# Kernel tuning notes

Measured on AMD Instinct MI355X. Metric: run time of the kernel, lower is better.

## Reference

```python
import jax, jax.numpy as jnp
import numpy as np

CHANNEL = 256
MEM_SIZE = 684
POS_NUM = 128
NEG_NUM = 512
TEMP = 1.0
CLASS_NUM = 60
BANK_ROWS = MEM_SIZE * CLASS_NUM  # 41040
BATCH = 512


def setup_inputs() -> dict:
    key = jax.random.key(0)
    k1, k2, k3, k4 = jax.random.split(key, 4)
    f = jax.random.normal(k1, (BATCH, CHANNEL), dtype=jnp.float32)
    f_normed = f / jnp.linalg.norm(f, axis=-1, keepdims=True)
    label = jax.random.randint(k2, (BATCH,), 0, CLASS_NUM, dtype=jnp.int32)
    bank = jax.random.normal(k3, (BANK_ROWS, CHANNEL), dtype=jnp.float32)
    bank = bank / jnp.linalg.norm(bank, axis=-1, keepdims=True)
    bank_flag = jnp.ones((BANK_ROWS,), dtype=jnp.float32)  # warmed-up bank
    rand_neg = jax.random.uniform(k4, (BATCH, BANK_ROWS), dtype=jnp.float32)
    # exact torch roundrobin enqueue logic (sequential over the batch)
    rr = np.zeros(CLASS_NUM, dtype=np.int64)
    idxs = []
    for i in np.asarray(label).tolist():
        rr[i] = rr[i] + 1 if rr[i] < CLASS_NUM - 1 else 0
        idxs.append(int(rr[i]) + i * MEM_SIZE)
    enqueue_idx = jnp.asarray(idxs, dtype=jnp.int32)
    return {"f_normed": f_normed, "label": label, "enqueue_idx": enqueue_idx,
            "bank": bank, "bank_flag": bank_flag, "rand_neg": rand_neg}


def reference(f_normed, label, enqueue_idx, bank, bank_flag, rand_neg):
    N = f_normed.shape[0]
    # enqueue (detached write, as in torch: Bank[indies] = f_normed.detach())
    bank = bank.at[enqueue_idx].set(jax.lax.stop_gradient(f_normed))
    flag = bank_flag.at[enqueue_idx].set(1.0)
    # all_pairs: [N, M]
    all_pairs = jnp.einsum('nc,mc->nm', f_normed, bank)
    bank_label = jnp.tile(jnp.arange(CLASS_NUM), MEM_SIZE)  # arange(C).repeat(mem)
    eq = label[:, None] == bank_label[None, :]
    valid = flag > 0
    pos_mask = eq & valid
    neg_mask = (~eq) & valid
    # hard positives: smallest POS_NUM positive similarities per row
    pos_hard = jnp.sort(jnp.where(pos_mask, all_pairs, jnp.inf), axis=-1)[:, :POS_NUM]
    # hard negatives: largest NEG_NUM negative similarities per row
    neg_hard, _ = jax.lax.top_k(jnp.where(neg_mask, all_pairs, -jnp.inf), NEG_NUM)
    # random negatives: uniform sample without replacement via noise argsort
    r = jnp.where(neg_mask, rand_neg, jnp.inf)
    rand_idx = jnp.argsort(r, axis=-1)[:, :NEG_NUM]
    neg_rand = jnp.take_along_axis(all_pairs, rand_idx, axis=-1)
    # combined logits: [N, 2*POS_NUM, 1+NEG_NUM]
    pos = pos_hard[:, :, None]
    h2h = jnp.concatenate([pos, jnp.broadcast_to(neg_hard[:, None, :], (N, POS_NUM, NEG_NUM))], axis=-1)
    h2r = jnp.concatenate([pos, jnp.broadcast_to(neg_rand[:, None, :], (N, POS_NUM, NEG_NUM))], axis=-1)
    combined = jnp.concatenate([h2h, h2r], axis=1).reshape(-1, 1 + NEG_NUM)
    # cross entropy with target class 0 for every row
    loss = -jnp.mean(jax.nn.log_softmax(combined / TEMP, axis=-1)[:, 0])
    return loss
```

## Files before the change

### kernel.cpp

```cpp
#include <hip/hip_runtime.h>

#define CH    256
#define MEM   684
#define POSN  128
#define NEGN  512
#define CLS   60
#define ROWS  41040
#define BATCHN 512

typedef unsigned int u32;
typedef unsigned short u16;
typedef unsigned long long u64;

typedef __attribute__((ext_vector_type(8))) short bf16x8;
typedef __attribute__((ext_vector_type(4))) float f32x4;

__device__ __forceinline__ float b2f(u16 u) { return __uint_as_float(((u32)u) << 16); }
__device__ __forceinline__ u16 f2b(float x) {
  u32 u = __float_as_uint(x);
  u32 r = ((u >> 16) & 1u) + 0x7FFFu;
  return (u16)((u + r) >> 16);
}
__device__ __forceinline__ u32 umin2(u32 a, u32 b) { return a < b ? a : b; }

#if defined(__has_builtin)
#if __has_builtin(__builtin_amdgcn_global_load_lds)
#define HAVE_GLL 1
#endif
#endif

__device__ __forceinline__ void stage16(const u16* g, u16* l) {
#ifdef HAVE_GLL
  __builtin_amdgcn_global_load_lds((const __attribute__((address_space(1))) void*)g,
                                   (__attribute__((address_space(3))) void*)l, 16, 0, 0);
#else
  *(uint4*)l = *(const uint4*)g;
#endif
}

__global__ __launch_bounds__(256) void k_convert(const float* __restrict__ bank,
                                                 u16* __restrict__ bankB) {
  size_t i = (size_t)(blockIdx.x * 256 + threadIdx.x) * 8;
  float4 a = *(const float4*)(bank + i);
  float4 b = *(const float4*)(bank + i + 4);
  uint4 o;
  o.x = (u32)f2b(a.x) | ((u32)f2b(a.y) << 16);
  o.y = (u32)f2b(a.z) | ((u32)f2b(a.w) << 16);
  o.z = (u32)f2b(b.x) | ((u32)f2b(b.y) << 16);
  o.w = (u32)f2b(b.z) | ((u32)f2b(b.w) << 16);
  *(uint4*)(bankB + i) = o;
}

__global__ __launch_bounds__(256) void k_scatter(const float* __restrict__ f,
                                                 const int* __restrict__ enq,
                                                 u16* __restrict__ fB,
                                                 u16* __restrict__ bankB) {
  int n = blockIdx.x, t = threadIdx.x;
  u16 v = f2b(f[n * CH + t]);
  fB[n * CH + t] = v;
  int row = enq[n];
  bankB[(size_t)row * CH + t] = v;
}

__global__ __launch_bounds__(256) void k_gemm(const u16* __restrict__ fB,
                                              const u16* __restrict__ bankB,
                                              u16* __restrict__ Cb) {
  __shared__ __align__(16) u16 As[2][128 * 32];
  __shared__ __align__(16) u16 Bs[2][128 * 32];
  const int tid = threadIdx.x;
  const int wave = tid >> 6, lane = tid & 63;

  const u32 id = blockIdx.x;
  const u32 q = 160u, r4 = 4u;
  const u32 xcd = id & 7u, jj = id >> 3;
  const u32 wg = (xcd < r4 ? xcd * (q + 1u) : r4 * (q + 1u) + (xcd - r4) * q) + jj;
  const int bm = (int)(wg & 3u) * 128;
  const int bn = (int)(wg >> 2) * 128;

  const int wm = (wave & 1) * 64, wn = (wave >> 1) * 64;
  const int m_in = lane & 15;
  const int ks = (lane >> 4) * 8;

  f32x4 acc[4][4] = {};

  auto STAGE = [&](int buf, int k0) {
#pragma unroll
    for (int i = 0; i < 2; i++) {
      int u = tid + 256 * i;
      int row = u >> 2;
      int kk = (u & 3) * 8;
      stage16(fB + (size_t)(bm + row) * CH + k0 + kk, &As[buf][u * 8]);
      int rb = bn + row;
      if (rb >= ROWS) rb = bn;
      stage16(bankB + (size_t)rb * CH + k0 + kk, &Bs[buf][u * 8]);
    }
  };

  STAGE(0, 0);
  __syncthreads();
  int cur = 0;
#pragma unroll 1
  for (int step = 0; step < CH / 32; step++) {
    if (step < CH / 32 - 1) STAGE(cur ^ 1, (step + 1) * 32);

    bf16x8 af[4], bf[4];
#pragma unroll
    for (int t4 = 0; t4 < 4; t4++) {
      af[t4] = *(const bf16x8*)(&As[cur][(wm + t4 * 16 + m_in) * 32 + ks]);
      bf[t4] = *(const bf16x8*)(&Bs[cur][(wn + t4 * 16 + m_in) * 32 + ks]);
    }
#pragma unroll
    for (int mi = 0; mi < 4; mi++)
#pragma unroll
      for (int ni = 0; ni < 4; ni++)
        acc[mi][ni] = __builtin_amdgcn_mfma_f32_16x16x32_bf16(bf[ni], af[mi], acc[mi][ni], 0, 0, 0);

    __syncthreads();
    cur ^= 1;
  }

  const int cc = lane & 15;
  const int rr = (lane >> 4) * 4;
#pragma unroll
  for (int mi = 0; mi < 4; mi++) {
    const int row = bm + wm + mi * 16 + cc;
#pragma unroll
    for (int ni = 0; ni < 4; ni++) {
      const int n0 = bn + wn + ni * 16 + rr;
      if (n0 < ROWS) {
        u64 pk = (u64)f2b(acc[mi][ni][0]) | ((u64)f2b(acc[mi][ni][1]) << 16) |
                 ((u64)f2b(acc[mi][ni][2]) << 32) | ((u64)f2b(acc[mi][ni][3]) << 48);
        *(u64*)(Cb + (size_t)row * ROWS + n0) = pk;
      }
    }
  }
}

__device__ __forceinline__ u32 wscan_incl(u32 v) {
  int lane = (int)(threadIdx.x & 63);
#pragma unroll
  for (int off = 1; off < 64; off <<= 1) {
    u32 t = __shfl_up(v, off, 64);
    if (lane >= off) v += t;
  }
  return v;
}

__device__ __forceinline__ u32 scan1024(u32 v, u32* tmp, int tid) {
  u32 inc = wscan_incl(v);
  int wid = tid >> 6;
  if ((tid & 63) == 63) tmp[wid] = inc;
  __syncthreads();
  if (tid < 64) {
    u32 t = (tid < 16) ? tmp[tid] : 0u;
    u32 ti = wscan_incl(t);
    if (tid < 16) tmp[tid] = ti - t;
  }
  __syncthreads();
  u32 r = inc + tmp[wid];
  __syncthreads();
  return r;
}

__device__ __forceinline__ float redsum1024(float v, float* tmp, int tid) {
#pragma unroll
  for (int off = 32; off > 0; off >>= 1) v += __shfl_xor(v, off, 64);
  int wid = tid >> 6;
  if ((tid & 63) == 0) tmp[wid] = v;
  __syncthreads();
  if (tid == 0) {
    float t = 0.f;
#pragma unroll
    for (int i = 0; i < 16; i++) t += tmp[i];
    tmp[0] = t;
  }
  __syncthreads();
  float r = tmp[0];
  __syncthreads();
  return r;
}

__device__ __forceinline__ int binof(float v, float lo, float scale) {
  int b = (int)((v - lo) * scale);
  return b < 0 ? 0 : (b > 2047 ? 2047 : b);
}

#define VITER 5
#define VTAIL 80
#define VTAILBASE 40960
#define CAPC 3072
#define CAPR 1536

__global__ __launch_bounds__(1024, 8) void k_select(const u16* __restrict__ Cb,
                                                    const float* __restrict__ rnd,
                                                    const int* __restrict__ label,
                                                    float* __restrict__ partial) {
  const int n = blockIdx.x;
  const int tid = threadIdx.x;
  const u16* crow = Cb + (size_t)n * ROWS;
  const float* rrow = rnd + (size_t)n * ROWS;
  const int lab = label[n];

  __shared__ __align__(16) char smem[56448];
  u32* histc = (u32*)(smem);
  u32* histr = (u32*)(smem + 8192);
  float* clist = (float*)(smem + 16384);
  float* rl_rv = (float*)(smem + 28672);
  float* rl_cv = (float*)(smem + 34816);
  u32* rl_mi = (u32*)(smem + 40960);
  u32* stmp = (u32*)(smem + 47104);
  float* fred = (float*)(smem + 47104);
  float* cb_c = (float*)(smem + 51200);
  float* rb_r = (float*)(smem + 53248);
  float* rb_c = (float*)(smem + 54272);
  u32* rb_m = (u32*)(smem + 55296);
  u32* ctl = (u32*)(smem + 56320);
  float* bc_f = (float*)(ctl + 8);

  const int rv0 = (tid * 8) % 60;

  float T1 = 0.09375f;
  float T0 = 0.03125f;
  u32 F = 0, G = 0;
  float sc_c, sc_r;

  for (int attempt = 0;; attempt++) {
    for (int i = tid; i < 2048; i += 1024) { histc[i] = 0; histr[i] = 0; }
    if (tid == 0) { ctl[0] = 0; ctl[1] = 0; }
    __syncthreads();
    sc_c = 2048.0f / (1.0625f - T1);
    sc_r = 2048.0f / T0;
    int rb = rv0;
    uint4 cr = *(const uint4*)(crow + tid * 8);
    float4 ra = *(const float4*)(rrow + tid * 8);
    float4 rb4 = *(const float4*)(rrow + tid * 8 + 4);
#pragma unroll 1
    for (int it = 0; it < VITER; it++) {
      int m8 = (it * 1024 + tid) * 8;
      uint4 crN;
      float4 raN, rbN;
      if (it + 1 < VITER) {
        int m8n = ((it + 1) * 1024 + tid) * 8;
        crN = *(const uint4*)(crow + m8n);
        raN = *(const float4*)(rrow + m8n);
        rbN = *(const float4*)(rrow + m8n + 4);
      }
      u32 cw[4] = {cr.x, cr.y, cr.z, cr.w};
      float rs[8] = {ra.x, ra.y, ra.z, ra.w, rb4.x, rb4.y, rb4.z, rb4.w};
      u32 mc = 0, mr = 0;
      int r = rb;
#pragma unroll
      for (int j = 0; j < 8; j++) {
        bool isneg = (r != lab);
        float c = b2f((u16)(cw[j >> 1] >> ((j & 1) * 16)));
        if (isneg && c > T1) mc |= (1u << j);
        if (isneg && rs[j] < T0) mr |= (1u << j);
        r++;
        if (r == 60) r = 0;
      }
      u32 s1 = 0, s2 = 0;
      if (mc) s1 = atomicAdd(&ctl[0], (u32)__popc(mc));
      if (mr) s2 = atomicAdd(&ctl[1], (u32)__popc(mr));
#pragma unroll
      for (int j = 0; j < 8; j++) {
        if (mc & (1u << j)) {
          float c = b2f((u16)(cw[j >> 1] >> ((j & 1) * 16)));
          if (s1 < CAPC) clist[s1] = c;
          atomicAdd(&histc[binof(c, T1, sc_c)], 1u);
          s1++;
        }
        if (mr & (1u << j)) {
          float c = b2f((u16)(cw[j >> 1] >> ((j & 1) * 16)));
          if (s2 < CAPR) { rl_rv[s2] = rs[j]; rl_cv[s2] = c; rl_mi[s2] = (u32)(m8 + j); }
          atomicAdd(&histr[binof(rs[j], 0.0f, sc_r)], 1u);
          s2++;
        }
      }
      cr = crN; ra = raN; rb4 = rbN;
      rb += 32;
      if (rb >= 60) rb -= 60;
    }
    if (tid < VTAIL) {
      int m = VTAILBASE + tid;
      int r = 40 + tid;
      if (r >= 60) r -= 60;
      bool isneg = (r != lab);
      float c = b2f(crow[m]);
      if (isneg && c > T1) {
        u32 s1 = atomicAdd(&ctl[0], 1u);
        if (s1 < CAPC) clist[s1] = c;
        atomicAdd(&histc[binof(c, T1, sc_c)], 1u);
      }
      float rv = rrow[m];
      if (isneg && rv < T0) {
        u32 s2 = atomicAdd(&ctl[1], 1u);
        if (s2 < CAPR) { rl_rv[s2] = rv; rl_cv[s2] = c; rl_mi[s2] = (u32)m; }
        atomicAdd(&histr[binof(rv, 0.0f, sc_r)], 1u);
      }
    }
    __syncthreads();
    F = ctl[0];
    G = ctl[1];
    __syncthreads();
    if (F >= NEGN && G >= NEGN) break;
    if (F < NEGN) T1 = -1.1f;
    if (G < NEGN) T0 = 1.1f;
  }
  const bool listc_ok = (F <= CAPC);
  const bool listr_ok = (G <= CAPR);

  if (tid == 0) { ctl[2] = 0; ctl[3] = 0; ctl[4] = 0; ctl[5] = 0; ctl[6] = 0; ctl[7] = 0; }
  u32 fsum = histc[tid * 2] + histc[tid * 2 + 1];
  u32 finc = scan1024(fsum, stmp, tid);
  u32 fexc = finc - fsum;
  u32 tcpos = F - NEGN + 1;
  if (fexc < tcpos && tcpos <= finc) {
    u32 run = fexc;
#pragma unroll
    for (int i = 0; i < 2; i++) {
      u32 h = histc[tid * 2 + i];
      if (run + h >= tcpos) { ctl[4] = (u32)(tid * 2 + i); ctl[5] = F - (run + h); break; }
      run += h;
    }
  }
  u32 gsum = histr[tid * 2] + histr[tid * 2 + 1];
  u32 ginc = scan1024(gsum, stmp, tid);
  u32 gexc = ginc - gsum;
  if (gexc < NEGN && NEGN <= ginc) {
    u32 run = gexc;
#pragma unroll
    for (int i = 0; i < 2; i++) {
      u32 h = histr[tid * 2 + i];
      if (run + h >= NEGN) { ctl[6] = (u32)(tid * 2 + i); ctl[7] = run; break; }
      run += h;
    }
  }
  __syncthreads();
  const u32 b_c = ctl[4], cnt_gt = ctl[5];
  const u32 b_r = ctl[6], cnt_lt = ctl[7];
  const u32 need_c = NEGN - cnt_gt;
  const u32 need_r = NEGN - cnt_lt;

  float sH = 0.f, sR = 0.f;
  if (listc_ok) {
    for (u32 i = tid; i < F; i += 1024) {
      float c = clist[i];
      u32 b = (u32)binof(c, T1, sc_c);
      if (b > b_c) sH += expf(c);
      else if (b == b_c) {
        u32 id = atomicAdd(&ctl[2], 1u);
        if (id < 512) cb_c[id] = c;
      }
    }
  }
  if (listr_ok) {
    for (u32 i = tid; i < G; i += 1024) {
      float rv = rl_rv[i];
      u32 b = (u32)binof(rv, 0.0f, sc_r);
      if (b < b_r) sR += expf(rl_cv[i]);
      else if (b == b_r) {
        u32 id = atomicAdd(&ctl[3], 1u);
        if (id < 256) { rb_r[id] = rv; rb_c[id] = rl_cv[i]; rb_m[id] = rl_mi[i]; }
      }
    }
  }
  if (!listc_ok || !listr_ok) {
    for (int m = tid; m < ROWS; m += 1024) {
      int r = m % 60;
      if (r == lab) continue;
      float c = b2f(crow[m]);
      if (!listc_ok && c > T1) {
        u32 b = (u32)binof(c, T1, sc_c);
        if (b > b_c) sH += expf(c);
        else if (b == b_c) {
          u32 id = atomicAdd(&ctl[2], 1u);
          if (id < 512) cb_c[id] = c;
        }
      }
      if (!listr_ok) {
        float rv = rrow[m];
        if (rv < T0) {
          u32 b = (u32)binof(rv, 0.0f, sc_r);
          if (b < b_r) sR += expf(c);
          else if (b == b_r) {
            u32 id = atomicAdd(&ctl[3], 1u);
            if (id < 256) { rb_r[id] = rv; rb_c[id] = c; rb_m[id] = (u32)m; }
          }
        }
      }
    }
  }
  __syncthreads();
  float SHsum = redsum1024(sH, fred, tid);
  float SRsum = redsum1024(sR, fred, tid);

  if (tid == 0) {
    float addH = 0.f;
    u32 Lc = umin2(ctl[2], 512u);
    u32 kc = umin2(need_c, Lc);
    for (u32 k = 0; k < kc; k++) {
      int best = 0;
      float bv = -3.0e38f;
      for (u32 i = 0; i < Lc; i++)
        if (cb_c[i] > bv) { bv = cb_c[i]; best = (int)i; }
      cb_c[best] = -3.0e38f;
      addH += expf(bv);
    }
    u32 Lr = umin2(ctl[3], 256u);
    for (u32 i = 1; i < Lr; i++) {
      float rv = rb_r[i]; u32 mm = rb_m[i]; float cv = rb_c[i];
      int j = (int)i - 1;
      while (j >= 0 && (rb_r[j] > rv || (rb_r[j] == rv && rb_m[j] > mm))) {
        rb_r[j + 1] = rb_r[j]; rb_m[j + 1] = rb_m[j]; rb_c[j + 1] = rb_c[j];
        j--;
      }
      rb_r[j + 1] = rv; rb_m[j + 1] = mm; rb_c[j + 1] = cv;
    }
    float addR = 0.f;
    u32 kr = umin2(need_r, Lr);
    for (u32 i = 0; i < kr; i++) addR += expf(rb_c[i]);
    bc_f[0] = addH;
    bc_f[1] = addR;
  }
  __syncthreads();
  const float S_H = SHsum + bc_f[0];
  const float S_R = SRsum + bc_f[1];
  __syncthreads();

  float pval = 0.f;
  int pbin = 0;
  const bool hasp = tid < MEM;
  const float PLO = -1.03125f;
  const float PSC = 2048.0f / 2.09375f;
  if (hasp) {
    pval = b2f(crow[lab + CLS * tid]);
    pbin = binof(pval, PLO, PSC);
  }
  for (int i = tid; i < 2048; i += 1024) histc[i] = 0;
  if (tid == 0) { ctl[2] = 0; ctl[4] = 0; ctl[5] = 0; }
  __syncthreads();
  if (hasp) atomicAdd(&histc[pbin], 1u);
  __syncthreads();
  u32 hsum = histc[tid * 2] + histc[tid * 2 + 1];
  u32 hinc = scan1024(hsum, stmp, tid);
  u32 hexc = hinc - hsum;
  if (hexc < POSN && POSN <= hinc) {
    u32 run = hexc;
#pragma unroll
    for (int i = 0; i < 2; i++) {
      u32 h = histc[tid * 2 + i];
      if (run + h >= POSN) { ctl[4] = (u32)(tid * 2 + i); ctl[5] = run; break; }
      run += h;
    }
  }
  __syncthreads();
  const u32 b_p = ctl[4], cnt_below = ctl[5];
  const u32 need_p = POSN - cnt_below;
  if (hasp && (u32)pbin == b_p) {
    u32 id = atomicAdd(&ctl[2], 1u);
    if (id < 512) cb_c[id] = pval;
  }
  float term = 0.f;
  if (hasp && (u32)pbin < b_p) {
    float e = expf(pval);
    term = (pval - logf(e + S_H)) + (pval - logf(e + S_R));
  }
  __syncthreads();
  if (tid == 0) {
    u32 L = umin2(ctl[2], 512u);
    u32 kp = umin2(need_p, L);
    float add = 0.f;
    for (u32 k = 0; k < kp; k++) {
      int best = 0;
      float bv = 3.0e38f;
      for (u32 i = 0; i < L; i++)
        if (cb_c[i] < bv) { bv = cb_c[i]; best = (int)i; }
      cb_c[best] = 3.0e38f;
      float e = expf(bv);
      add += (bv - logf(e + S_H)) + (bv - logf(e + S_R));
    }
    bc_f[0] = add;
  }
  __syncthreads();
  float tot = redsum1024(term, fred, tid);
  if (tid == 0) partial[n] = tot + bc_f[0];
}

__global__ __launch_bounds__(256) void k_final(const float* __restrict__ partial,
                                               float* __restrict__ out) {
  __shared__ float fred[256];
  int tid = threadIdx.x;
  float v = partial[tid] + partial[tid + 256];
  fred[tid] = v;
  __syncthreads();
  for (int off = 128; off > 0; off >>= 1) {
    if (tid < off) fred[tid] += fred[tid + off];
    __syncthreads();
  }
  if (tid == 0) out[0] = -fred[0] / (float)(BATCHN * 2 * POSN);
}

extern "C" void kernel_launch(void* const* d_in, const int* in_sizes, int n_in,
                              void* d_out, int out_size, void* d_ws, size_t ws_size,
                              hipStream_t stream) {
  const float* f = (const float*)d_in[0];
  const int* label = (const int*)d_in[1];
  const int* enq = (const int*)d_in[2];
  const float* bank = (const float*)d_in[3];
  const float* rnd = (const float*)d_in[5];
  float* out = (float*)d_out;

  char* ws = (char*)d_ws;
  u16* bankB = (u16*)ws;
  u16* fB = (u16*)(ws + 21012480);
  u16* Cb = (u16*)(ws + 21012480 + 262144);
  float* partial = (float*)(ws + 21012480 + 262144 + 42024960);

  k_convert<<<dim3(5130), dim3(256), 0, stream>>>(bank, bankB);
  k_scatter<<<dim3(BATCHN), dim3(256), 0, stream>>>(f, enq, fB, bankB);
  k_gemm<<<dim3(1284), dim3(256), 0, stream>>>(fB, bankB, Cb);
  k_select<<<dim3(BATCHN), dim3(1024), 0, stream>>>(Cb, rnd, label, partial);
  k_final<<<dim3(1), dim3(256), 0, stream>>>(partial, out);
}
```

Before: 241.5 us.

## Split candidate filtering into a separate two-blocks-per-row prep kernel

Adds a k_prep kernel that scans each row's similarities and random values in two halves (1024 blocks), compacting threshold-passing candidates, their random keys and the positive-class entries into global buffers. k_select then builds its histograms and sums from these compact lists when they fit the per-half caps, and falls back to the original full scan otherwise. The aim is more parallelism for the bandwidth-heavy filtering pass and less work inside the 512 large select blocks. The cost is an extra launch plus global writes and re-reads of the candidate lists.

```diff
diff --git a/kernel.cpp b/kernel.cpp
--- a/kernel.cpp
+++ b/kernel.cpp
@@ -185,6 +185,111 @@
   return b < 0 ? 0 : (b > 2047 ? 2047 : b);
 }
 
+#define HALF  20520
+#define HC    1792
+#define HR    768
+#define T1BASE 0.09375f
+#define T0BASE 0.03125f
+
+__global__ __launch_bounds__(512) void k_prep(const u16* __restrict__ Cb,
+                                              const float* __restrict__ rnd,
+                                              const int* __restrict__ label,
+                                              u32* __restrict__ cnt_c,
+                                              u32* __restrict__ cnt_r,
+                                              u16* __restrict__ clist_g,
+                                              float* __restrict__ rrv_g,
+                                              u16* __restrict__ rcv_g,
+                                              u32* __restrict__ rmi_g,
+                                              u16* __restrict__ pos_g) {
+  const int bid = blockIdx.x;
+  const int n = bid >> 1, h = bid & 1;
+  const int tid = threadIdx.x;
+  const u16* crow = Cb + (size_t)n * ROWS;
+  const float* rrow = rnd + (size_t)n * ROWS;
+  const int lab = label[n];
+  const int m0 = h * HALF;
+
+  __shared__ u16 lc[HC];
+  __shared__ float lrv[HR];
+  __shared__ u16 lcv[HR];
+  __shared__ u32 lmi[HR];
+  __shared__ u32 cnt[2];
+  if (tid < 2) cnt[tid] = 0;
+  __syncthreads();
+
+#pragma unroll 1
+  for (int it = 0; it < 5; it++) {
+    int m8 = m0 + (it * 512 + tid) * 8;
+    uint4 cr = *(const uint4*)(crow + m8);
+    float4 ra = *(const float4*)(rrow + m8);
+    float4 rb4 = *(const float4*)(rrow + m8 + 4);
+    u32 cw[4] = {cr.x, cr.y, cr.z, cr.w};
+    float rs[8] = {ra.x, ra.y, ra.z, ra.w, rb4.x, rb4.y, rb4.z, rb4.w};
+    int r = m8 % 60;
+    u32 mc = 0, mr = 0;
+#pragma unroll
+    for (int j = 0; j < 8; j++) {
+      u16 cu = (u16)(cw[j >> 1] >> ((j & 1) * 16));
+      if (r == lab) {
+        pos_g[n * MEM + (m8 + j - lab) / 60] = cu;
+      } else {
+        float c = b2f(cu);
+        if (c > T1BASE) mc |= (1u << j);
+        if (rs[j] < T0BASE) mr |= (1u << j);
+      }
+      r++;
+      if (r == 60) r = 0;
+    }
+    u32 s1 = 0, s2 = 0;
+    if (mc) s1 = atomicAdd(&cnt[0], (u32)__popc(mc));
+    if (mr) s2 = atomicAdd(&cnt[1], (u32)__popc(mr));
+#pragma unroll
+    for (int j = 0; j < 8; j++) {
+      if (mc & (1u << j)) {
+        if (s1 < HC) lc[s1] = (u16)(cw[j >> 1] >> ((j & 1) * 16));
+        s1++;
+      }
+      if (mr & (1u << j)) {
+        if (s2 < HR) {
+          lrv[s2] = rs[j];
+          lcv[s2] = (u16)(cw[j >> 1] >> ((j & 1) * 16));
+          lmi[s2] = (u32)(m8 + j);
+        }
+        s2++;
+      }
+    }
+  }
+  if (tid < 40) {
+    int m = m0 + 20480 + tid;
+    u16 cu = crow[m];
+    int r = m % 60;
+    if (r == lab) {
+      pos_g[n * MEM + (m - lab) / 60] = cu;
+    } else {
+      float c = b2f(cu);
+      if (c > T1BASE) {
+        u32 s = atomicAdd(&cnt[0], 1u);
+        if (s < HC) lc[s] = cu;
+      }
+      float rv = rrow[m];
+      if (rv < T0BASE) {
+        u32 s = atomicAdd(&cnt[1], 1u);
+        if (s < HR) { lrv[s] = rv; lcv[s] = cu; lmi[s] = (u32)m; }
+      }
+    }
+  }
+  __syncthreads();
+  const int idx = n * 2 + h;
+  u32 c0 = cnt[0], c1 = cnt[1];
+  if (tid == 0) { cnt_c[idx] = c0; cnt_r[idx] = c1; }
+  for (u32 i = tid; i < umin2(c0, (u32)HC); i += 512) clist_g[(size_t)idx * HC + i] = lc[i];
+  for (u32 i = tid; i < umin2(c1, (u32)HR); i += 512) {
+    rrv_g[(size_t)idx * HR + i] = lrv[i];
+    rcv_g[(size_t)idx * HR + i] = lcv[i];
+    rmi_g[(size_t)idx * HR + i] = lmi[i];
+  }
+}
+
 #define VITER 5
 #define VTAIL 80
 #define VTAILBASE 40960
@@ -194,6 +299,13 @@
 __global__ __launch_bounds__(1024, 8) void k_select(const u16* __restrict__ Cb,
                                                     const float* __restrict__ rnd,
                                                     const int* __restrict__ label,
+                                                    const u32* __restrict__ cnt_c,
+                                                    const u32* __restrict__ cnt_r,
+                                                    const u16* __restrict__ clist_g,
+                                                    const float* __restrict__ rrv_g,
+                                                    const u16* __restrict__ rcv_g,
+                                                    const u32* __restrict__ rmi_g,
+                                                    const u16* __restrict__ pos_g,
                                                     float* __restrict__ partial) {
   const int n = blockIdx.x;
   const int tid = threadIdx.x;
@@ -217,97 +329,113 @@
   u32* ctl = (u32*)(smem + 56320);
   float* bc_f = (float*)(ctl + 8);
 
-  const int rv0 = (tid * 8) % 60;
-
-  float T1 = 0.09375f;
-  float T0 = 0.03125f;
+  float T1 = T1BASE;
+  float T0 = T0BASE;
   u32 F = 0, G = 0;
   float sc_c, sc_r;
-
-  for (int attempt = 0;; attempt++) {
+  bool listc_ok = true, listr_ok = true;
+
+  const u32 cc0 = cnt_c[n * 2], cc1 = cnt_c[n * 2 + 1];
+  const u32 rc0 = cnt_r[n * 2], rc1 = cnt_r[n * 2 + 1];
+  F = cc0 + cc1;
+  G = rc0 + rc1;
+  const bool fast = (cc0 <= HC && cc1 <= HC && rc0 <= HR && rc1 <= HR &&
+                     F >= NEGN && G >= NEGN);
+  sc_c = 2048.0f / (1.0625f - T1);
+  sc_r = 2048.0f / T0;
+
+  if (fast) {
     for (int i = tid; i < 2048; i += 1024) { histc[i] = 0; histr[i] = 0; }
-    if (tid == 0) { ctl[0] = 0; ctl[1] = 0; }
     __syncthreads();
-    sc_c = 2048.0f / (1.0625f - T1);
-    sc_r = 2048.0f / T0;
-    int rb = rv0;
-    uint4 cr = *(const uint4*)(crow + tid * 8);
-    float4 ra = *(const float4*)(rrow + tid * 8);
-    float4 rb4 = *(const float4*)(rrow + tid * 8 + 4);
 #pragma unroll 1
-    for (int it = 0; it < VITER; it++) {
-      int m8 = (it * 1024 + tid) * 8;
-      uint4 crN;
-      float4 raN, rbN;
-      if (it + 1 < VITER) {
-        int m8n = ((it + 1) * 1024 + tid) * 8;
-        crN = *(const uint4*)(crow + m8n);
-        raN = *(const float4*)(rrow + m8n);
-        rbN = *(const float4*)(rrow + m8n + 4);
-      }
-      u32 cw[4] = {cr.x, cr.y, cr.z, cr.w};
-      float rs[8] = {ra.x, ra.y, ra.z, ra.w, rb4.x, rb4.y, rb4.z, rb4.w};
-      u32 mc = 0, mr = 0;
-      int r = rb;
-#pragma unroll
-      for (int j = 0; j < 8; j++) {
+    for (int hh = 0; hh < 2; hh++) {
+      const int idx = n * 2 + hh;
+      const u32 cc = hh ? cc1 : cc0;
+      for (u32 i = tid; i < cc; i += 1024)
+        atomicAdd(&histc[binof(b2f(clist_g[(size_t)idx * HC + i]), T1, sc_c)], 1u);
+      const u32 rc = hh ? rc1 : rc0;
+      for (u32 i = tid; i < rc; i += 1024)
+        atomicAdd(&histr[binof(rrv_g[(size_t)idx * HR + i], 0.0f, sc_r)], 1u);
+    }
+    __syncthreads();
+  } else {
+    const int rv0 = (tid * 8) % 60;
+    for (int attempt = 0;; attempt++) {
+      for (int i = tid; i < 2048; i += 1024) { histc[i] = 0; histr[i] = 0; }
+      if (tid == 0) { ctl[0] = 0; ctl[1] = 0; }
+      __syncthreads();
+      sc_c = 2048.0f / (1.0625f - T1);
+      sc_r = 2048.0f / T0;
+      int rb = rv0;
+#pragma unroll 1
+      for (int it = 0; it < VITER; it++) {
+        int m8 = (it * 1024 + tid) * 8;
+        uint4 cr = *(const uint4*)(crow + m8);
+        float4 ra = *(const float4*)(rrow + m8);
+        float4 rb4 = *(const float4*)(rrow + m8 + 4);
+        u32 cw[4] = {cr.x, cr.y, cr.z, cr.w};
+        float rs[8] = {ra.x, ra.y, ra.z, ra.w, rb4.x, rb4.y, rb4.z, rb4.w};
+        u32 mc = 0, mr = 0;
+        int r = rb;
+#pragma unroll
+        for (int j = 0; j < 8; j++) {
+          bool isneg = (r != lab);
+          float c = b2f((u16)(cw[j >> 1] >> ((j & 1) * 16)));
+          if (isneg && c > T1) mc |= (1u << j);
+          if (isneg && rs[j] < T0) mr |= (1u << j);
+          r++;
+          if (r == 60) r = 0;
+        }
+        u32 s1 = 0, s2 = 0;
+        if (mc) s1 = atomicAdd(&ctl[0], (u32)__popc(mc));
+        if (mr) s2 = atomicAdd(&ctl[1], (u32)__popc(mr));
+#pragma unroll
+        for (int j = 0; j < 8; j++) {
+          if (mc & (1u << j)) {
+            float c = b2f((u16)(cw[j >> 1] >> ((j & 1) * 16)));
+            if (s1 < CAPC) clist[s1] = c;
+            atomicAdd(&histc[binof(c, T1, sc_c)], 1u);
+            s1++;
+          }
+          if (mr & (1u << j)) {
+            float c = b2f((u16)(cw[j >> 1] >> ((j & 1) * 16)));
+            if (s2 < CAPR) { rl_rv[s2] = rs[j]; rl_cv[s2] = c; rl_mi[s2] = (u32)(m8 + j); }
+            atomicAdd(&histr[binof(rs[j], 0.0f, sc_r)], 1u);
+            s2++;
+          }
+        }
+        rb += 32;
+        if (rb >= 60) rb -= 60;
+      }
+      if (tid < VTAIL) {
+        int m = VTAILBASE + tid;
+        int r = 40 + tid;
+        if (r >= 60) r -= 60;
         bool isneg = (r != lab);
-        float c = b2f((u16)(cw[j >> 1] >> ((j & 1) * 16)));
-        if (isneg && c > T1) mc |= (1u << j);
-        if (isneg && rs[j] < T0) mr |= (1u << j);
-        r++;
-        if (r == 60) r = 0;
-      }
-      u32 s1 = 0, s2 = 0;
-      if (mc) s1 = atomicAdd(&ctl[0], (u32)__popc(mc));
-      if (mr) s2 = atomicAdd(&ctl[1], (u32)__popc(mr));
-#pragma unroll
-      for (int j = 0; j < 8; j++) {
-        if (mc & (1u << j)) {
-          float c = b2f((u16)(cw[j >> 1] >> ((j & 1) * 16)));
+        float c = b2f(crow[m]);
+        if (isneg && c > T1) {
+          u32 s1 = atomicAdd(&ctl[0], 1u);
           if (s1 < CAPC) clist[s1] = c;
           atomicAdd(&histc[binof(c, T1, sc_c)], 1u);
-          s1++;
-        }
-        if (mr & (1u << j)) {
-          float c = b2f((u16)(cw[j >> 1] >> ((j & 1) * 16)));
-          if (s2 < CAPR) { rl_rv[s2] = rs[j]; rl_cv[s2] = c; rl_mi[s2] = (u32)(m8 + j); }
-          atomicAdd(&histr[binof(rs[j], 0.0f, sc_r)], 1u);
-          s2++;
-        }
-      }
-      cr = crN; ra = raN; rb4 = rbN;
-      rb += 32;
-      if (rb >= 60) rb -= 60;
-    }
-    if (tid < VTAIL) {
-      int m = VTAILBASE + tid;
-      int r = 40 + tid;
-      if (r >= 60) r -= 60;
-      bool isneg = (r != lab);
-      float c = b2f(crow[m]);
-      if (isneg && c > T1) {
-        u32 s1 = atomicAdd(&ctl[0], 1u);
-        if (s1 < CAPC) clist[s1] = c;
-        atomicAdd(&histc[binof(c, T1, sc_c)], 1u);
-      }
-      float rv = rrow[m];
-      if (isneg && rv < T0) {
-        u32 s2 = atomicAdd(&ctl[1], 1u);
-        if (s2 < CAPR) { rl_rv[s2] = rv; rl_cv[s2] = c; rl_mi[s2] = (u32)m; }
-        atomicAdd(&histr[binof(rv, 0.0f, sc_r)], 1u);
-      }
-    }
-    __syncthreads();
-    F = ctl[0];
-    G = ctl[1];
-    __syncthreads();
-    if (F >= NEGN && G >= NEGN) break;
-    if (F < NEGN) T1 = -1.1f;
-    if (G < NEGN) T0 = 1.1f;
-  }
-  const bool listc_ok = (F <= CAPC);
-  const bool listr_ok = (G <= CAPR);
+        }
+        float rv = rrow[m];
+        if (isneg && rv < T0) {
+          u32 s2 = atomicAdd(&ctl[1], 1u);
+          if (s2 < CAPR) { rl_rv[s2] = rv; rl_cv[s2] = c; rl_mi[s2] = (u32)m; }
+          atomicAdd(&histr[binof(rv, 0.0f, sc_r)], 1u);
+        }
+      }
+      __syncthreads();
+      F = ctl[0];
+      G = ctl[1];
+      __syncthreads();
+      if (F >= NEGN && G >= NEGN) break;
+      if (F < NEGN) T1 = -1.1f;
+      if (G < NEGN) T0 = 1.1f;
+    }
+    listc_ok = (F <= CAPC);
+    listr_ok = (G <= CAPR);
+  }
 
   if (tid == 0) { ctl[2] = 0; ctl[3] = 0; ctl[4] = 0; ctl[5] = 0; ctl[6] = 0; ctl[7] = 0; }
   u32 fsum = histc[tid * 2] + histc[tid * 2 + 1];
@@ -342,34 +470,13 @@
   const u32 need_r = NEGN - cnt_lt;
 
   float sH = 0.f, sR = 0.f;
-  if (listc_ok) {
-    for (u32 i = tid; i < F; i += 1024) {
-      float c = clist[i];
-      u32 b = (u32)binof(c, T1, sc_c);
-      if (b > b_c) sH += expf(c);
-      else if (b == b_c) {
-        u32 id = atomicAdd(&ctl[2], 1u);
-        if (id < 512) cb_c[id] = c;
-      }
-    }
-  }
-  if (listr_ok) {
-    for (u32 i = tid; i < G; i += 1024) {
-      float rv = rl_rv[i];
-      u32 b = (u32)binof(rv, 0.0f, sc_r);
-      if (b < b_r) sR += expf(rl_cv[i]);
-      else if (b == b_r) {
-        u32 id = atomicAdd(&ctl[3], 1u);
-        if (id < 256) { rb_r[id] = rv; rb_c[id] = rl_cv[i]; rb_m[id] = rl_mi[i]; }
-      }
-    }
-  }
-  if (!listc_ok || !listr_ok) {
-    for (int m = tid; m < ROWS; m += 1024) {
-      int r = m % 60;
-      if (r == lab) continue;
-      float c = b2f(crow[m]);
-      if (!listc_ok && c > T1) {
+  if (fast) {
+#pragma unroll 1
+    for (int hh = 0; hh < 2; hh++) {
+      const int idx = n * 2 + hh;
+      const u32 cc = hh ? cc1 : cc0;
+      for (u32 i = tid; i < cc; i += 1024) {
+        float c = b2f(clist_g[(size_t)idx * HC + i]);
         u32 b = (u32)binof(c, T1, sc_c);
         if (b > b_c) sH += expf(c);
         else if (b == b_c) {
@@ -377,14 +484,66 @@
           if (id < 512) cb_c[id] = c;
         }
       }
-      if (!listr_ok) {
-        float rv = rrow[m];
-        if (rv < T0) {
-          u32 b = (u32)binof(rv, 0.0f, sc_r);
-          if (b < b_r) sR += expf(c);
-          else if (b == b_r) {
-            u32 id = atomicAdd(&ctl[3], 1u);
-            if (id < 256) { rb_r[id] = rv; rb_c[id] = c; rb_m[id] = (u32)m; }
+      const u32 rc = hh ? rc1 : rc0;
+      for (u32 i = tid; i < rc; i += 1024) {
+        float rv = rrv_g[(size_t)idx * HR + i];
+        u32 b = (u32)binof(rv, 0.0f, sc_r);
+        if (b < b_r) sR += expf(b2f(rcv_g[(size_t)idx * HR + i]));
+        else if (b == b_r) {
+          u32 id = atomicAdd(&ctl[3], 1u);
+          if (id < 256) {
+            rb_r[id] = rv;
+            rb_c[id] = b2f(rcv_g[(size_t)idx * HR + i]);
+            rb_m[id] = rmi_g[(size_t)idx * HR + i];
+          }
+        }
+      }
+    }
+  } else {
+    if (listc_ok) {
+      for (u32 i = tid; i < F; i += 1024) {
+        float c = clist[i];
+        u32 b = (u32)binof(c, T1, sc_c);
+        if (b > b_c) sH += expf(c);
+        else if (b == b_c) {
+          u32 id = atomicAdd(&ctl[2], 1u);
+          if (id < 512) cb_c[id] = c;
+        }
+      }
+    }
+    if (listr_ok) {
+      for (u32 i = tid; i < G; i += 1024) {
+        float rv = rl_rv[i];
+        u32 b = (u32)binof(rv, 0.0f, sc_r);
+        if (b < b_r) sR += expf(rl_cv[i]);
+        else if (b == b_r) {
+          u32 id = atomicAdd(&ctl[3], 1u);
+          if (id < 256) { rb_r[id] = rv; rb_c[id] = rl_cv[i]; rb_m[id] = rl_mi[i]; }
+        }
+      }
+    }
+    if (!listc_ok || !listr_ok) {
+      for (int m = tid; m < ROWS; m += 1024) {
+        int r = m % 60;
+        if (r == lab) continue;
+        float c = b2f(crow[m]);
+        if (!listc_ok && c > T1) {
+          u32 b = (u32)binof(c, T1, sc_c);
+          if (b > b_c) sH += expf(c);
+          else if (b == b_c) {
+            u32 id = atomicAdd(&ctl[2], 1u);
+            if (id < 512) cb_c[id] = c;
+          }
+        }
+        if (!listr_ok) {
+          float rv = rrow[m];
+          if (rv < T0) {
+            u32 b = (u32)binof(rv, 0.0f, sc_r);
+            if (b < b_r) sR += expf(c);
+            else if (b == b_r) {
+              u32 id = atomicAdd(&ctl[3], 1u);
+              if (id < 256) { rb_r[id] = rv; rb_c[id] = c; rb_m[id] = (u32)m; }
+            }
           }
         }
       }
@@ -433,7 +592,7 @@
   const float PLO = -1.03125f;
   const float PSC = 2048.0f / 2.09375f;
   if (hasp) {
-    pval = b2f(crow[lab + CLS * tid]);
+    pval = b2f(pos_g[n * MEM + tid]);
     pbin = binof(pval, PLO, PSC);
   }
   for (int i = tid; i < 2048; i += 1024) histc[i] = 0;
@@ -513,12 +672,23 @@
   char* ws = (char*)d_ws;
   u16* bankB = (u16*)ws;
   u16* fB = (u16*)(ws + 21012480);
-  u16* Cb = (u16*)(ws + 21012480 + 262144);
-  float* partial = (float*)(ws + 21012480 + 262144 + 42024960);
+  u16* Cb = (u16*)(ws + 21274624);
+  float* partial = (float*)(ws + 63299584);
+  u32* cnt_c = (u32*)(ws + 63301632);
+  u32* cnt_r = (u32*)(ws + 63305728);
+  u16* clist_g = (u16*)(ws + 63309824);
+  float* rrv_g = (float*)(ws + 66979840);
+  u16* rcv_g = (u16*)(ws + 70125568);
+  u32* rmi_g = (u32*)(ws + 71698432);
+  u16* pos_g = (u16*)(ws + 74844160);
 
   k_convert<<<dim3(5130), dim3(256), 0, stream>>>(bank, bankB);
   k_scatter<<<dim3(BATCHN), dim3(256), 0, stream>>>(f, enq, fB, bankB);
   k_gemm<<<dim3(1284), dim3(256), 0, stream>>>(fB, bankB, Cb);
-  k_select<<<dim3(BATCHN), dim3(1024), 0, stream>>>(Cb, rnd, label, partial);
+  k_prep<<<dim3(1024), dim3(512), 0, stream>>>(Cb, rnd, label, cnt_c, cnt_r,
+                                               clist_g, rrv_g, rcv_g, rmi_g, pos_g);
+  k_select<<<dim3(BATCHN), dim3(1024), 0, stream>>>(Cb, rnd, label, cnt_c, cnt_r,
+                                                    clist_g, rrv_g, rcv_g, rmi_g, pos_g,
+                                                    partial);
   k_final<<<dim3(1), dim3(256), 0, stream>>>(partial, out);
 }
```

After: 252.3 us. 4.5% more time.
